# Kernel tuning notes

Hardware: AMD Instinct MI355X
Metric: run time of the kernel (lower is better)

Reference implementation:

```python
import jax, jax.numpy as jnp
import numpy as np

EPS = 1e-5

def _conv3x3(x, w, b):
    # x: [B,C,H,W], w: [O,I,3,3], b: [O]; padding=1 preserves HxW
    y = jax.lax.conv_general_dilated(
        x, w, window_strides=(1, 1), padding=((1, 1), (1, 1)),
        dimension_numbers=('NCHW', 'OIHW', 'NCHW'))
    return y + b[None, :, None, None]

def _instance_norm(x):
    # InstanceNorm2d(affine=False): normalize over spatial dims per (sample, channel)
    mu = jnp.mean(x, axis=(2, 3), keepdims=True)
    var = jnp.var(x, axis=(2, 3), keepdims=True)
    return (x - mu) * jax.lax.rsqrt(var + EPS)

def setup_inputs() -> dict:
    key = jax.random.key(0)
    k1, k2, k3 = jax.random.split(key, 3)
    B, Cin, Cout, H, W = 8, 32, 64, 320, 320
    x = jax.random.normal(k1, (B, Cin, H, W), dtype=jnp.float32)
    w1 = jax.random.normal(k2, (Cout, Cin, 3, 3), dtype=jnp.float32) * (1.0 / np.sqrt(Cin * 9))
    b1 = jnp.zeros((Cout,), dtype=jnp.float32)
    w2 = jax.random.normal(k3, (Cout, Cout, 3, 3), dtype=jnp.float32) * (1.0 / np.sqrt(Cout * 9))
    b2 = jnp.zeros((Cout,), dtype=jnp.float32)
    return {"x": x, "w1": w1, "b1": b1, "w2": w2, "b2": b2}

def reference(x, w1, b1, w2, b2):
    # conv1 -> InstanceNorm -> ReLU -> (Dropout p=0 identity)
    h = jax.nn.relu(_instance_norm(_conv3x3(x, w1, b1)))
    # conv2 -> InstanceNorm -> ReLU -> (Dropout p=0 identity)
    out = jax.nn.relu(_instance_norm(_conv3x3(h, w2, b2)))
    return out
```

## Files before the change

### kernel.cpp

```cpp
#include <hip/hip_runtime.h>

#define HH 320
#define WW 320
#define BB 8
static constexpr float EPS = 1e-5f;

typedef __attribute__((ext_vector_type(8))) short bf16x8;
typedef __attribute__((ext_vector_type(4))) float f32x4;

__device__ inline float bf2f(unsigned short u) {
    union { unsigned int i; float f; } v; v.i = ((unsigned int)u) << 16; return v.f;
}
__device__ inline unsigned short f2bf(float f) {
    union { float f; unsigned int i; } v; v.f = f;
    unsigned int r = v.i + 0x7fffu + ((v.i >> 16) & 1u);
    return (unsigned short)(r >> 16);
}
__device__ inline void glds16(const void* g, void* l) {
    __builtin_amdgcn_global_load_lds(
        (const __attribute__((address_space(1))) unsigned int*)g,
        (__attribute__((address_space(3))) unsigned int*)l, 16, 0, 0);
}

__global__ __launch_bounds__(256) void prep_hwc(const float* __restrict__ in,
                                                unsigned short* __restrict__ out)
{
    __shared__ float sT[32][65];
    const int tid = threadIdx.x;
    const int x0  = blockIdx.x * 64;
    const int y   = blockIdx.y;
    const int b   = blockIdx.z;
    for (int e = tid; e < 32 * 64; e += 256) {
        int c = e >> 6, x = e & 63;
        sT[c][x] = in[(((size_t)(b * 32 + c) * HH) + y) * WW + x0 + x];
    }
    __syncthreads();
    for (int e = tid; e < 64 * 32; e += 256) {
        int x = e >> 5, c = e & 31;
        out[((((size_t)b * HH + y) * WW) + x0 + x) * 32 + c] = f2bf(sT[c][x]);
    }
}

__global__ __launch_bounds__(256) void wprep_swz(const float* __restrict__ w1,
                                                 const float* __restrict__ w2,
                                                 unsigned short* __restrict__ wt1,
                                                 unsigned short* __restrict__ wt2)
{
    int i = blockIdx.x * 256 + threadIdx.x;
    if (i < 2304) {
        int s = i & 3, oc = (i >> 2) & 63, kk = i >> 8;
        int icq = s ^ ((oc >> 1) & 3);
        const float* src = w1 + ((size_t)oc * 32 + icq * 8) * 9 + kk;
        unsigned short pk[8];
#pragma unroll
        for (int j = 0; j < 8; ++j) pk[j] = f2bf(src[j * 9]);
        *(bf16x8*)&wt1[(size_t)i * 8] = *(bf16x8*)pk;
    }
    if (i < 4608) {
        int icc = i / 2304, u = i - icc * 2304;
        int s = u & 3, oc = (u >> 2) & 63, kk = u >> 8;
        int icq = s ^ ((oc >> 1) & 3);
        const float* src = w2 + ((size_t)oc * 64 + icc * 32 + icq * 8) * 9 + kk;
        unsigned short pk[8];
#pragma unroll
        for (int j = 0; j < 8; ++j) pk[j] = f2bf(src[j * 9]);
        *(bf16x8*)&wt2[(size_t)i * 8] = *(bf16x8*)pk;
    }
}

template<int CIN, int NORM>
__global__ __launch_bounds__(256, 2) void conv_mfma(
    const unsigned short* __restrict__ in_hwc,
    const float2* __restrict__ stats_in,
    const unsigned short* __restrict__ wt,
    const float* __restrict__ bias,
    unsigned short* __restrict__ out_hwc,
    float2* __restrict__ partials)
{
    constexpr int ICC = CIN / 32;

    __shared__ __align__(16) unsigned short sA[6 * 264 * 8];
    __shared__ __align__(16) unsigned short sW[2304 * 8];
    __shared__ float sRedS[256];
    __shared__ float sRedSS[256];
    __shared__ float2 sStats[64];

    const int tid = threadIdx.x;
    const int x0  = blockIdx.x * 64;
    const int y0  = blockIdx.y * 4;
    const int b   = blockIdx.z;
    const int w   = tid >> 6;
    const int l   = tid & 63;
    const int lm  = l & 15;
    const int g   = l >> 4;

    if (NORM) {
        if (tid < 64) sStats[tid] = stats_in[b * 64 + tid];
    }

    f32x4 acc[4][4];
#pragma unroll
    for (int fx = 0; fx < 4; ++fx)
#pragma unroll
        for (int fn = 0; fn < 4; ++fn)
            acc[fx][fn] = (f32x4){0.f, 0.f, 0.f, 0.f};

    for (int icc = 0; icc < ICC; ++icc) {
        __syncthreads();

        {
            const unsigned short* wsrc = wt + (size_t)icc * 2304 * 8;
            const int base = w * 576;
#pragma unroll
            for (int i = 0; i < 9; ++i)
                glds16(wsrc + (size_t)(base + i * 64 + l) * 8,
                       sW + (size_t)(base + i * 64) * 8);
        }

        if (NORM == 0) {
            for (int r = w; r < 6; r += 4) {
                int gy = y0 + r - 1;
                unsigned short* ldsrow = sA + r * 2112;
                if ((unsigned)gy < HH) {
                    const unsigned short* rowbase =
                        in_hwc + ((size_t)(b * HH + gy) * WW) * CIN + icc * 32;
#pragma unroll
                    for (int i = 0; i < 4; ++i) {
                        int u  = 4 + i * 64 + l;
                        int x  = u >> 2;
                        int cs = (u & 3) ^ ((x >> 1) & 3);
                        glds16(rowbase + (size_t)(x0 + x - 1) * CIN + cs * 8,
                               ldsrow + (size_t)(4 + i * 64) * 8);
                    }
                } else {
                    for (int u2 = l; u2 < 264; u2 += 64)
                        *(bf16x8*)(ldsrow + u2 * 8) = (bf16x8){0,0,0,0,0,0,0,0};
                }
            }
            if (tid < 48) {
                int icq = tid & 3, side = (tid >> 2) & 1, r = tid >> 3;
                int xs = side ? 65 : 0;
                int gy = y0 + r - 1, gx = x0 + xs - 1;
                bf16x8 v = (bf16x8){0,0,0,0,0,0,0,0};
                if ((unsigned)gy < HH && (unsigned)gx < WW)
                    v = *(const bf16x8*)&in_hwc[(((size_t)(b * HH + gy) * WW) + gx) * CIN + icc * 32 + icq * 8];
                *(bf16x8*)&sA[(r * 264 + xs * 4 + icq) * 8] = v;
            }
        } else {
#pragma unroll
            for (int k = 0; k < 7; ++k) {
                int e = tid + k * 256;
                if (e < 1584) {
                    int r = e / 264, rem = e - r * 264;
                    int x = rem >> 2, icq = rem & 3;
                    int gy = y0 + r - 1, gx = x0 + x - 1;
                    bf16x8 v = (bf16x8){0,0,0,0,0,0,0,0};
                    if ((unsigned)gy < HH && (unsigned)gx < WW)
                        v = *(const bf16x8*)&in_hwc[(((size_t)(b * HH + gy) * WW) + gx) * CIN + icc * 32 + icq * 8];
                    unsigned short res[8];
#pragma unroll
                    for (int j = 0; j < 8; ++j) {
                        float2 ms = sStats[icc * 32 + icq * 8 + j];
                        res[j] = f2bf(fmaxf((bf2f(((unsigned short*)&v)[j]) - ms.x) * ms.y, 0.f));
                    }
                    *(bf16x8*)&sA[(r * 264 + x * 4 + (icq ^ ((x >> 1) & 3))) * 8] = *(bf16x8*)res;
                }
            }
        }
        __syncthreads();

#pragma unroll
        for (int kk = 0; kk < 9; ++kk) {
            const int ky = kk / 3, kx = kk - ky * 3;
            bf16x8 af[4], bfr[4];
#pragma unroll
            for (int fx = 0; fx < 4; ++fx) {
                int xl = fx * 16 + lm + kx;
                int u  = (xl * 4 + g) ^ ((xl >> 1) & 3);
                af[fx] = *(const bf16x8*)&sA[((w + ky) * 264 + u) * 8];
            }
#pragma unroll
            for (int fn = 0; fn < 4; ++fn) {
                int ocr = fn * 16 + lm;
                int p   = (kk * 64 + ocr) * 4 + (g ^ ((ocr >> 1) & 3));
                bfr[fn] = *(const bf16x8*)&sW[p * 8];
            }
#pragma unroll
            for (int fn = 0; fn < 4; ++fn)
#pragma unroll
                for (int fx = 0; fx < 4; ++fx)
                    acc[fx][fn] = __builtin_amdgcn_mfma_f32_16x16x32_bf16(
                        bfr[fn], af[fx], acc[fx][fn], 0, 0, 0);
        }
    }

    const int row = y0 + w;
#pragma unroll
    for (int fo = 0; fo < 4; ++fo) {
        float4 b4 = *(const float4*)&bias[fo * 16 + g * 4];
        float bb[4] = {b4.x, b4.y, b4.z, b4.w};
        float sj[4] = {0,0,0,0}, qj[4] = {0,0,0,0};
#pragma unroll
        for (int fp = 0; fp < 4; ++fp) {
            unsigned short pk[4];
#pragma unroll
            for (int j = 0; j < 4; ++j) {
                float v = acc[fp][fo][j] + bb[j];
                sj[j] += v; qj[j] += v * v;
                pk[j] = f2bf(v);
            }
            *(short4*)&out_hwc[(((size_t)b * HH + row) * WW + x0 + fp * 16 + lm) * 64 + fo * 16 + g * 4] =
                *(short4*)pk;
        }
#pragma unroll
        for (int m = 1; m <= 8; m <<= 1)
#pragma unroll
            for (int j = 0; j < 4; ++j) {
                sj[j] += __shfl_xor(sj[j], m);
                qj[j] += __shfl_xor(qj[j], m);
            }
        if (lm == 0) {
#pragma unroll
            for (int j = 0; j < 4; ++j) {
                sRedS [w * 64 + fo * 16 + g * 4 + j] = sj[j];
                sRedSS[w * 64 + fo * 16 + g * 4 + j] = qj[j];
            }
        }
    }
    __syncthreads();
    if (tid < 64) {
        float S = 0.f, SS = 0.f;
#pragma unroll
        for (int q = 0; q < 4; ++q) { S += sRedS[q * 64 + tid]; SS += sRedSS[q * 64 + tid]; }
        partials[((size_t)b * 400 + blockIdx.y * 5 + blockIdx.x) * 64 + tid] = make_float2(S, SS);
    }
}

__global__ __launch_bounds__(256) void reduce_stats(const float2* __restrict__ partials,
                                                    float2* __restrict__ stats)
{
    const int b  = blockIdx.x;
    const int oc = threadIdx.x & 63;
    const int q  = threadIdx.x >> 6;
    float s = 0.f, ss = 0.f;
    for (int i = q; i < 400; i += 4) {
        float2 p = partials[((size_t)b * 400 + i) * 64 + oc];
        s += p.x; ss += p.y;
    }
    __shared__ float2 red[4][64];
    red[q][oc] = make_float2(s, ss);
    __syncthreads();
    if (threadIdx.x < 64) {
        float S = 0.f, SS = 0.f;
#pragma unroll
        for (int k = 0; k < 4; ++k) { S += red[k][threadIdx.x].x; SS += red[k][threadIdx.x].y; }
        const float n = (float)(HH * WW);
        float mean = S / n;
        float var  = fmaxf(SS / n - mean * mean, 0.f);
        stats[b * 64 + threadIdx.x] = make_float2(mean, rsqrtf(var + EPS));
    }
}

__global__ __launch_bounds__(256) void finalize_t(const unsigned short* __restrict__ h2,
                                                  const float2* __restrict__ stats,
                                                  float* __restrict__ out)
{
    __shared__ float2 sSt[64];
    const int tid = threadIdx.x;
    const int b   = blockIdx.z;
    if (tid < 64) sSt[tid] = stats[b * 64 + tid];
    __syncthreads();
    const int r   = tid >> 6;
    const int px  = tid & 63;
    const int row = blockIdx.y * 4 + r;
    const int x   = blockIdx.x * 64 + px;
    const unsigned short* src = h2 + ((size_t)(b * HH + row) * WW + x) * 64;
    bf16x8 v[8];
#pragma unroll
    for (int cq = 0; cq < 8; ++cq) v[cq] = *(const bf16x8*)(src + cq * 8);
#pragma unroll
    for (int cq = 0; cq < 8; ++cq)
#pragma unroll
        for (int j = 0; j < 8; ++j) {
            int c = cq * 8 + j;
            float2 ms = sSt[c];
            float f = fmaxf((bf2f(((unsigned short*)&v[cq])[j]) - ms.x) * ms.y, 0.f);
            out[((size_t)(b * 64 + c) * HH + row) * WW + x] = f;
        }
}

extern "C" void kernel_launch(void* const* d_in, const int* in_sizes, int n_in,
                              void* d_out, int out_size, void* d_ws, size_t ws_size,
                              hipStream_t stream)
{
    const float* x  = (const float*)d_in[0];
    const float* w1 = (const float*)d_in[1];
    const float* b1 = (const float*)d_in[2];
    const float* w2 = (const float*)d_in[3];
    const float* b2 = (const float*)d_in[4];
    float* out = (float*)d_out;

    char* ws = (char*)d_ws;
    unsigned short* h    = (unsigned short*)ws;
    float2* partials     = (float2*)(ws + 104857600);
    float2* stats1       = (float2*)(ws + 104857600 + 1638400);
    float2* stats2       = (float2*)(ws + 104857600 + 1638400 + 4096);
    unsigned short* reg2 = (unsigned short*)(ws + 104857600 + 1638400 + 8192);
    unsigned short* x_hwc = reg2;
    unsigned short* h2    = reg2;

    unsigned short* wt2 = (unsigned short*)((char*)d_out + 209715200 - 73728);
    unsigned short* wt1 = (unsigned short*)((char*)d_out + 209715200 - 73728 - 36864);

    dim3 cgrid(5, 80, BB);

    wprep_swz<<<18, 256, 0, stream>>>(w1, w2, wt1, wt2);
    prep_hwc<<<dim3(5, HH, BB), 256, 0, stream>>>(x, x_hwc);

    conv_mfma<32, 0><<<cgrid, 256, 0, stream>>>(x_hwc, nullptr, wt1, b1, h, partials);
    reduce_stats<<<BB, 256, 0, stream>>>(partials, stats1);
    conv_mfma<64, 1><<<cgrid, 256, 0, stream>>>(h, stats1, wt2, b2, h2, partials);
    reduce_stats<<<BB, 256, 0, stream>>>(partials, stats2);
    finalize_t<<<dim3(5, 80, BB), 256, 0, stream>>>(h2, stats2, out);
}
```

Baseline: 339.7 us.

## Add ring-buffered conv1 kernel processing 16 rows per block with row reuse

Adds a dedicated conv1 kernel in which each block computes 16 output rows using a 10-slot LDS ring of input rows. Weights are loaded once per block, and each new 4-row step stages only the rows it still needs while computing the current ones. This replaces the 4-row-per-block conv1, which reloaded 6 input rows and the full weight tile for every block. The trade-offs are a quarter as many blocks (800), a larger LDS footprint, and a reduce_stats call that now takes the partial count as a parameter.

```diff
diff --git a/kernel.cpp b/kernel.cpp
--- a/kernel.cpp
+++ b/kernel.cpp
@@ -68,6 +68,165 @@
     }
 }
 
+__global__ __launch_bounds__(256, 2) void conv1_ring(
+    const unsigned short* __restrict__ in_hwc,
+    const unsigned short* __restrict__ wt,
+    const float* __restrict__ bias,
+    unsigned short* __restrict__ out_hwc,
+    float2* __restrict__ partials)
+{
+    __shared__ __align__(16) unsigned short sA[10 * 264 * 8];
+    __shared__ __align__(16) unsigned short sW[2304 * 8];
+    __shared__ float sRedS[256];
+    __shared__ float sRedSS[256];
+
+    const int tid = threadIdx.x;
+    const int x0  = blockIdx.x * 64;
+    const int yb  = blockIdx.y * 16;
+    const int b   = blockIdx.z;
+    const int w   = tid >> 6;
+    const int l   = tid & 63;
+    const int lm  = l & 15;
+    const int g   = l >> 4;
+
+    {
+        const int base = w * 576;
+#pragma unroll
+        for (int i = 0; i < 9; ++i)
+            glds16(wt + (size_t)(base + i * 64 + l) * 8,
+                   sW + (size_t)(base + i * 64) * 8);
+    }
+
+    auto stage_row = [&](int rl, int slot) {
+        int gy = yb - 1 + rl;
+        unsigned short* ldsrow = sA + slot * 2112;
+        if ((unsigned)gy < HH) {
+            const unsigned short* rowbase = in_hwc + ((size_t)(b * HH + gy) * WW) * 32;
+#pragma unroll
+            for (int i = 0; i < 4; ++i) {
+                int u  = 4 + i * 64 + l;
+                int x  = u >> 2;
+                int cs = (u & 3) ^ ((x >> 1) & 3);
+                glds16(rowbase + (size_t)(x0 + x - 1) * 32 + cs * 8,
+                       ldsrow + (size_t)(4 + i * 64) * 8);
+            }
+            if (l < 8) {
+                int icq = l & 3, side = l >> 2;
+                int xs = side ? 65 : 0;
+                int gx = x0 + xs - 1;
+                bf16x8 v = (bf16x8){0,0,0,0,0,0,0,0};
+                if ((unsigned)gx < WW)
+                    v = *(const bf16x8*)&in_hwc[(((size_t)(b * HH + gy) * WW) + gx) * 32 + icq * 8];
+                *(bf16x8*)(ldsrow + (xs * 4 + icq) * 8) = v;
+            }
+        } else {
+            for (int u2 = l; u2 < 264; u2 += 64)
+                *(bf16x8*)(ldsrow + u2 * 8) = (bf16x8){0,0,0,0,0,0,0,0};
+        }
+    };
+
+    f32x4 acc[4][4];
+#pragma unroll
+    for (int fp = 0; fp < 4; ++fp)
+#pragma unroll
+        for (int fo = 0; fo < 4; ++fo)
+            acc[fp][fo] = (f32x4){0.f, 0.f, 0.f, 0.f};
+
+    float bb[4][4];
+#pragma unroll
+    for (int fo = 0; fo < 4; ++fo) {
+        float4 b4 = *(const float4*)&bias[fo * 16 + g * 4];
+        bb[fo][0] = b4.x; bb[fo][1] = b4.y; bb[fo][2] = b4.z; bb[fo][3] = b4.w;
+    }
+    float sjA[4][4] = {}, qjA[4][4] = {};
+
+    stage_row(w, w);
+    if (w < 2) stage_row(4 + w, 4 + w);
+    __syncthreads();
+
+    auto step = [&](int t, bool do_stage) {
+        if (do_stage) {
+            int rl = 4 * (t + 1) + 2 + w;
+            int slot = rl - (rl >= 10 ? 10 : 0);
+            stage_row(rl, slot);
+        }
+#pragma unroll
+        for (int kk = 0; kk < 9; ++kk) {
+            const int ky = kk / 3, kx = kk - ky * 3;
+            int rl = 4 * t + w + ky;
+            int slot = rl - (rl >= 10 ? 10 : 0);
+            const unsigned short* rowp = sA + slot * 2112;
+            bf16x8 af[4], bfr[4];
+#pragma unroll
+            for (int fp = 0; fp < 4; ++fp) {
+                int xl = fp * 16 + lm + kx;
+                int u  = (xl * 4 + g) ^ ((xl >> 1) & 3);
+                af[fp] = *(const bf16x8*)(rowp + u * 8);
+            }
+#pragma unroll
+            for (int fo = 0; fo < 4; ++fo) {
+                int ocr = fo * 16 + lm;
+                int p   = (kk * 64 + ocr) * 4 + (g ^ ((ocr >> 1) & 3));
+                bfr[fo] = *(const bf16x8*)&sW[p * 8];
+            }
+#pragma unroll
+            for (int fo = 0; fo < 4; ++fo)
+#pragma unroll
+                for (int fp = 0; fp < 4; ++fp)
+                    acc[fp][fo] = __builtin_amdgcn_mfma_f32_16x16x32_bf16(
+                        bfr[fo], af[fp], acc[fp][fo], 0, 0, 0);
+        }
+        const int row = yb + 4 * t + w;
+#pragma unroll
+        for (int fo = 0; fo < 4; ++fo) {
+#pragma unroll
+            for (int fp = 0; fp < 4; ++fp) {
+                unsigned short pk[4];
+#pragma unroll
+                for (int j = 0; j < 4; ++j) {
+                    float v = acc[fp][fo][j] + bb[fo][j];
+                    sjA[fo][j] += v; qjA[fo][j] += v * v;
+                    pk[j] = f2bf(v);
+                }
+                *(short4*)&out_hwc[(((size_t)b * HH + row) * WW + x0 + fp * 16 + lm) * 64 + fo * 16 + g * 4] =
+                    *(short4*)pk;
+                acc[fp][fo] = (f32x4){0.f, 0.f, 0.f, 0.f};
+            }
+        }
+        __syncthreads();
+    };
+
+    step(0, true);
+    step(1, true);
+    step(2, true);
+    step(3, false);
+
+#pragma unroll
+    for (int fo = 0; fo < 4; ++fo) {
+#pragma unroll
+        for (int m = 1; m <= 8; m <<= 1)
+#pragma unroll
+            for (int j = 0; j < 4; ++j) {
+                sjA[fo][j] += __shfl_xor(sjA[fo][j], m);
+                qjA[fo][j] += __shfl_xor(qjA[fo][j], m);
+            }
+        if (lm == 0) {
+#pragma unroll
+            for (int j = 0; j < 4; ++j) {
+                sRedS [w * 64 + fo * 16 + g * 4 + j] = sjA[fo][j];
+                sRedSS[w * 64 + fo * 16 + g * 4 + j] = qjA[fo][j];
+            }
+        }
+    }
+    __syncthreads();
+    if (tid < 64) {
+        float S = 0.f, SS = 0.f;
+#pragma unroll
+        for (int q = 0; q < 4; ++q) { S += sRedS[q * 64 + tid]; SS += sRedSS[q * 64 + tid]; }
+        partials[((size_t)b * 100 + blockIdx.y * 5 + blockIdx.x) * 64 + tid] = make_float2(S, SS);
+    }
+}
+
 template<int CIN, int NORM>
 __global__ __launch_bounds__(256, 2) void conv_mfma(
     const unsigned short* __restrict__ in_hwc,
@@ -107,7 +266,6 @@
 
     for (int icc = 0; icc < ICC; ++icc) {
         __syncthreads();
-
         {
             const unsigned short* wsrc = wt + (size_t)icc * 2304 * 8;
             const int base = w * 576;
@@ -116,7 +274,6 @@
                 glds16(wsrc + (size_t)(base + i * 64 + l) * 8,
                        sW + (size_t)(base + i * 64) * 8);
         }
-
         if (NORM == 0) {
             for (int r = w; r < 6; r += 4) {
                 int gy = y0 + r - 1;
@@ -198,14 +355,14 @@
 #pragma unroll
     for (int fo = 0; fo < 4; ++fo) {
         float4 b4 = *(const float4*)&bias[fo * 16 + g * 4];
-        float bb[4] = {b4.x, b4.y, b4.z, b4.w};
+        float bbv[4] = {b4.x, b4.y, b4.z, b4.w};
         float sj[4] = {0,0,0,0}, qj[4] = {0,0,0,0};
 #pragma unroll
         for (int fp = 0; fp < 4; ++fp) {
             unsigned short pk[4];
 #pragma unroll
             for (int j = 0; j < 4; ++j) {
-                float v = acc[fp][fo][j] + bb[j];
+                float v = acc[fp][fo][j] + bbv[j];
                 sj[j] += v; qj[j] += v * v;
                 pk[j] = f2bf(v);
             }
@@ -237,14 +394,14 @@
 }
 
 __global__ __launch_bounds__(256) void reduce_stats(const float2* __restrict__ partials,
-                                                    float2* __restrict__ stats)
+                                                    float2* __restrict__ stats, int count)
 {
     const int b  = blockIdx.x;
     const int oc = threadIdx.x & 63;
     const int q  = threadIdx.x >> 6;
     float s = 0.f, ss = 0.f;
-    for (int i = q; i < 400; i += 4) {
-        float2 p = partials[((size_t)b * 400 + i) * 64 + oc];
+    for (int i = q; i < count; i += 4) {
+        float2 p = partials[((size_t)b * count + i) * 64 + oc];
         s += p.x; ss += p.y;
     }
     __shared__ float2 red[4][64];
@@ -312,14 +469,12 @@
     unsigned short* wt2 = (unsigned short*)((char*)d_out + 209715200 - 73728);
     unsigned short* wt1 = (unsigned short*)((char*)d_out + 209715200 - 73728 - 36864);
 
-    dim3 cgrid(5, 80, BB);
-
     wprep_swz<<<18, 256, 0, stream>>>(w1, w2, wt1, wt2);
     prep_hwc<<<dim3(5, HH, BB), 256, 0, stream>>>(x, x_hwc);
 
-    conv_mfma<32, 0><<<cgrid, 256, 0, stream>>>(x_hwc, nullptr, wt1, b1, h, partials);
-    reduce_stats<<<BB, 256, 0, stream>>>(partials, stats1);
-    conv_mfma<64, 1><<<cgrid, 256, 0, stream>>>(h, stats1, wt2, b2, h2, partials);
-    reduce_stats<<<BB, 256, 0, stream>>>(partials, stats2);
+    conv1_ring<<<dim3(5, 20, BB), 256, 0, stream>>>(x_hwc, wt1, b1, h, partials);
+    reduce_stats<<<BB, 256, 0, stream>>>(partials, stats1, 100);
+    conv_mfma<64, 1><<<dim3(5, 80, BB), 256, 0, stream>>>(h, stats1, wt2, b2, h2, partials);
+    reduce_stats<<<BB, 256, 0, stream>>>(partials, stats2, 400);
     finalize_t<<<dim3(5, 80, BB), 256, 0, stream>>>(h2, stats2, out);
 }
```

Measured after the change: 332.6 us. 2.1% less time.

## Fold instance-norm scale into per-sample conv2 weights and split weight staging by kernel row

Applied to the files above, without the earlier changes.

Adds a wfold kernel that scales conv2 weights by each input channel's inverse std for each sample and folds the mean into a per-sample bias. Conv2's input transform then reduces to max(x, mu), with out-of-bounds padding set to mu, which removes the subtract and multiply per element. The conv kernel now stages weights one kernel row at a time, shrinking LDS use so launch bounds can rise to 4 blocks per CU; it also adds s_setprio around the MFMA loops and uses packed bf16 conversions. The cost is per-sample weight copies, extra barriers per input-channel chunk, and extra rounding because the folded weights are re-quantised to bf16.

```diff
diff --git a/kernel.cpp b/kernel.cpp
--- a/kernel.cpp
+++ b/kernel.cpp
@@ -15,6 +15,11 @@
     union { float f; unsigned int i; } v; v.f = f;
     unsigned int r = v.i + 0x7fffu + ((v.i >> 16) & 1u);
     return (unsigned short)(r >> 16);
+}
+__device__ inline unsigned int cvtpk(float a, float b) {
+    unsigned int r;
+    asm volatile("v_cvt_pk_bf16_f32 %0, %1, %2" : "=v"(r) : "v"(a), "v"(b));
+    return r;
 }
 __device__ inline void glds16(const void* g, void* l) {
     __builtin_amdgcn_global_load_lds(
@@ -68,8 +73,50 @@
     }
 }
 
+__global__ __launch_bounds__(256) void wfold(const unsigned short* __restrict__ wt2,
+                                             const float* __restrict__ b2,
+                                             const float2* __restrict__ stats1,
+                                             unsigned short* __restrict__ wt2b,
+                                             float* __restrict__ bias2b)
+{
+    __shared__ float sMu[64], sR[64];
+    __shared__ float sBias[256];
+    const int b = blockIdx.x, tid = threadIdx.x;
+    if (tid < 64) {
+        float2 ms = stats1[b * 64 + tid];
+        sMu[tid] = bf2f(f2bf(ms.x));
+        sR[tid]  = ms.y;
+    }
+    __syncthreads();
+    const int oc = tid & 63, rep = tid >> 6;
+    float bsum = 0.f;
+    for (int cs = rep * 2; cs < rep * 2 + 2; ++cs) {
+        int icc = cs >> 2, s = cs & 3;
+        int icq = s ^ ((oc >> 1) & 3);
+        for (int kk = 0; kk < 9; ++kk) {
+            size_t u = (size_t)icc * 2304 + kk * 256 + oc * 4 + s;
+            bf16x8 v = *(const bf16x8*)&wt2[u * 8];
+            unsigned short o8[8];
+#pragma unroll
+            for (int j = 0; j < 8; ++j) {
+                int ic = icc * 32 + icq * 8 + j;
+                unsigned short wb = f2bf(bf2f(((unsigned short*)&v)[j]) * sR[ic]);
+                o8[j] = wb;
+                bsum += bf2f(wb) * sMu[ic];
+            }
+            *(bf16x8*)&wt2b[((size_t)b * 4608 + u) * 8] = *(bf16x8*)o8;
+        }
+    }
+    sBias[tid] = bsum;
+    __syncthreads();
+    if (tid < 64) {
+        float t = sBias[tid] + sBias[tid + 64] + sBias[tid + 128] + sBias[tid + 192];
+        bias2b[b * 64 + tid] = b2[tid] - t;
+    }
+}
+
 template<int CIN, int NORM>
-__global__ __launch_bounds__(256, 2) void conv_mfma(
+__global__ __launch_bounds__(256, 4) void conv_mfma(
     const unsigned short* __restrict__ in_hwc,
     const float2* __restrict__ stats_in,
     const unsigned short* __restrict__ wt,
@@ -79,11 +126,13 @@
 {
     constexpr int ICC = CIN / 32;
 
-    __shared__ __align__(16) unsigned short sA[6 * 264 * 8];
-    __shared__ __align__(16) unsigned short sW[2304 * 8];
-    __shared__ float sRedS[256];
-    __shared__ float sRedSS[256];
-    __shared__ float2 sStats[64];
+    __shared__ __align__(16) char smem[38912];
+    unsigned short* sA    = (unsigned short*)smem;
+    unsigned short* sW    = (unsigned short*)(smem + 25344);
+    float*          sMaxMu= (float*)(smem + 37632);
+    unsigned short* sMuBf = (unsigned short*)(smem + 37888);
+    float* sRedS  = (float*)smem;
+    float* sRedSS = (float*)(smem + 1024);
 
     const int tid = threadIdx.x;
     const int x0  = blockIdx.x * 64;
@@ -94,28 +143,27 @@
     const int lm  = l & 15;
     const int g   = l >> 4;
 
+    const unsigned short* wtb = NORM ? wt + (size_t)b * 4608 * 8 : wt;
+    const float* biasb        = NORM ? bias + b * 64 : bias;
+
     if (NORM) {
-        if (tid < 64) sStats[tid] = stats_in[b * 64 + tid];
+        if (tid < 64) {
+            float2 ms = stats_in[b * 64 + tid];
+            unsigned short mb = f2bf(ms.x);
+            sMuBf[tid]  = mb;
+            sMaxMu[tid] = bf2f(mb);
+        }
     }
 
     f32x4 acc[4][4];
 #pragma unroll
-    for (int fx = 0; fx < 4; ++fx)
-#pragma unroll
-        for (int fn = 0; fn < 4; ++fn)
-            acc[fx][fn] = (f32x4){0.f, 0.f, 0.f, 0.f};
+    for (int fp = 0; fp < 4; ++fp)
+#pragma unroll
+        for (int fo = 0; fo < 4; ++fo)
+            acc[fp][fo] = (f32x4){0.f, 0.f, 0.f, 0.f};
 
     for (int icc = 0; icc < ICC; ++icc) {
         __syncthreads();
-
-        {
-            const unsigned short* wsrc = wt + (size_t)icc * 2304 * 8;
-            const int base = w * 576;
-#pragma unroll
-            for (int i = 0; i < 9; ++i)
-                glds16(wsrc + (size_t)(base + i * 64 + l) * 8,
-                       sW + (size_t)(base + i * 64) * 8);
-        }
 
         if (NORM == 0) {
             for (int r = w; r < 6; r += 4) {
@@ -154,63 +202,83 @@
                     int r = e / 264, rem = e - r * 264;
                     int x = rem >> 2, icq = rem & 3;
                     int gy = y0 + r - 1, gx = x0 + x - 1;
-                    bf16x8 v = (bf16x8){0,0,0,0,0,0,0,0};
-                    if ((unsigned)gy < HH && (unsigned)gx < WW)
-                        v = *(const bf16x8*)&in_hwc[(((size_t)(b * HH + gy) * WW) + gx) * CIN + icc * 32 + icq * 8];
-                    unsigned short res[8];
-#pragma unroll
-                    for (int j = 0; j < 8; ++j) {
-                        float2 ms = sStats[icc * 32 + icq * 8 + j];
-                        res[j] = f2bf(fmaxf((bf2f(((unsigned short*)&v)[j]) - ms.x) * ms.y, 0.f));
+                    int c0 = icc * 32 + icq * 8;
+                    unsigned int w4[4];
+                    if ((unsigned)gy < HH && (unsigned)gx < WW) {
+                        bf16x8 v = *(const bf16x8*)&in_hwc[(((size_t)(b * HH + gy) * WW) + gx) * CIN + c0];
+#pragma unroll
+                        for (int jp = 0; jp < 4; ++jp) {
+                            float f0 = fmaxf(bf2f(((unsigned short*)&v)[2 * jp]),     sMaxMu[c0 + 2 * jp]);
+                            float f1 = fmaxf(bf2f(((unsigned short*)&v)[2 * jp + 1]), sMaxMu[c0 + 2 * jp + 1]);
+                            w4[jp] = cvtpk(f0, f1);
+                        }
+                    } else {
+#pragma unroll
+                        for (int jp = 0; jp < 4; ++jp)
+                            w4[jp] = (unsigned int)sMuBf[c0 + 2 * jp] |
+                                     ((unsigned int)sMuBf[c0 + 2 * jp + 1] << 16);
                     }
-                    *(bf16x8*)&sA[(r * 264 + x * 4 + (icq ^ ((x >> 1) & 3))) * 8] = *(bf16x8*)res;
+                    *(uint4*)&sA[(r * 264 + x * 4 + (icq ^ ((x >> 1) & 3))) * 8] =
+                        make_uint4(w4[0], w4[1], w4[2], w4[3]);
                 }
             }
         }
-        __syncthreads();
-
-#pragma unroll
-        for (int kk = 0; kk < 9; ++kk) {
-            const int ky = kk / 3, kx = kk - ky * 3;
-            bf16x8 af[4], bfr[4];
-#pragma unroll
-            for (int fx = 0; fx < 4; ++fx) {
-                int xl = fx * 16 + lm + kx;
-                int u  = (xl * 4 + g) ^ ((xl >> 1) & 3);
-                af[fx] = *(const bf16x8*)&sA[((w + ky) * 264 + u) * 8];
-            }
-#pragma unroll
-            for (int fn = 0; fn < 4; ++fn) {
-                int ocr = fn * 16 + lm;
-                int p   = (kk * 64 + ocr) * 4 + (g ^ ((ocr >> 1) & 3));
-                bfr[fn] = *(const bf16x8*)&sW[p * 8];
-            }
-#pragma unroll
-            for (int fn = 0; fn < 4; ++fn)
-#pragma unroll
-                for (int fx = 0; fx < 4; ++fx)
-                    acc[fx][fn] = __builtin_amdgcn_mfma_f32_16x16x32_bf16(
-                        bfr[fn], af[fx], acc[fx][fn], 0, 0, 0);
-        }
-    }
+
+#pragma unroll
+        for (int kt = 0; kt < 3; ++kt) {
+            if (kt > 0) __syncthreads();
+            {
+                const unsigned short* wsrc = wtb + ((size_t)icc * 2304 + kt * 768) * 8;
+#pragma unroll
+                for (int k = 0; k < 3; ++k)
+                    glds16(wsrc + (size_t)(k * 256 + w * 64 + l) * 8,
+                           sW + (size_t)(k * 256 + w * 64) * 8);
+            }
+            __syncthreads();
+
+            __builtin_amdgcn_s_setprio(1);
+#pragma unroll
+            for (int kx = 0; kx < 3; ++kx) {
+                bf16x8 af[4], bfr[4];
+#pragma unroll
+                for (int fp = 0; fp < 4; ++fp) {
+                    int xl = fp * 16 + lm + kx;
+                    int u  = (xl * 4 + g) ^ ((xl >> 1) & 3);
+                    af[fp] = *(const bf16x8*)&sA[((w + kt) * 264 + u) * 8];
+                }
+#pragma unroll
+                for (int fo = 0; fo < 4; ++fo) {
+                    int ocr = fo * 16 + lm;
+                    int p   = (kx * 64 + ocr) * 4 + (g ^ ((ocr >> 1) & 3));
+                    bfr[fo] = *(const bf16x8*)&sW[p * 8];
+                }
+#pragma unroll
+                for (int fo = 0; fo < 4; ++fo)
+#pragma unroll
+                    for (int fp = 0; fp < 4; ++fp)
+                        acc[fp][fo] = __builtin_amdgcn_mfma_f32_16x16x32_bf16(
+                            bfr[fo], af[fp], acc[fp][fo], 0, 0, 0);
+            }
+            __builtin_amdgcn_s_setprio(0);
+        }
+    }
+
+    __syncthreads();
 
     const int row = y0 + w;
 #pragma unroll
     for (int fo = 0; fo < 4; ++fo) {
-        float4 b4 = *(const float4*)&bias[fo * 16 + g * 4];
+        float4 b4 = *(const float4*)&biasb[fo * 16 + g * 4];
         float bb[4] = {b4.x, b4.y, b4.z, b4.w};
         float sj[4] = {0,0,0,0}, qj[4] = {0,0,0,0};
 #pragma unroll
         for (int fp = 0; fp < 4; ++fp) {
-            unsigned short pk[4];
-#pragma unroll
-            for (int j = 0; j < 4; ++j) {
-                float v = acc[fp][fo][j] + bb[j];
-                sj[j] += v; qj[j] += v * v;
-                pk[j] = f2bf(v);
-            }
-            *(short4*)&out_hwc[(((size_t)b * HH + row) * WW + x0 + fp * 16 + lm) * 64 + fo * 16 + g * 4] =
-                *(short4*)pk;
+            float v0 = acc[fp][fo][0] + bb[0], v1 = acc[fp][fo][1] + bb[1];
+            float v2 = acc[fp][fo][2] + bb[2], v3 = acc[fp][fo][3] + bb[3];
+            sj[0] += v0; qj[0] += v0 * v0;  sj[1] += v1; qj[1] += v1 * v1;
+            sj[2] += v2; qj[2] += v2 * v2;  sj[3] += v3; qj[3] += v3 * v3;
+            uint2 st = make_uint2(cvtpk(v0, v1), cvtpk(v2, v3));
+            *(uint2*)&out_hwc[(((size_t)b * HH + row) * WW + x0 + fp * 16 + lm) * 64 + fo * 16 + g * 4] = st;
         }
 #pragma unroll
         for (int m = 1; m <= 8; m <<= 1)
@@ -237,14 +305,14 @@
 }
 
 __global__ __launch_bounds__(256) void reduce_stats(const float2* __restrict__ partials,
-                                                    float2* __restrict__ stats)
+                                                    float2* __restrict__ stats, int count)
 {
     const int b  = blockIdx.x;
     const int oc = threadIdx.x & 63;
     const int q  = threadIdx.x >> 6;
     float s = 0.f, ss = 0.f;
-    for (int i = q; i < 400; i += 4) {
-        float2 p = partials[((size_t)b * 400 + i) * 64 + oc];
+    for (int i = q; i < count; i += 4) {
+        float2 p = partials[((size_t)b * count + i) * 64 + oc];
         s += p.x; ss += p.y;
     }
     __shared__ float2 red[4][64];
@@ -309,8 +377,11 @@
     unsigned short* x_hwc = reg2;
     unsigned short* h2    = reg2;
 
-    unsigned short* wt2 = (unsigned short*)((char*)d_out + 209715200 - 73728);
-    unsigned short* wt1 = (unsigned short*)((char*)d_out + 209715200 - 73728 - 36864);
+    char* ob = (char*)d_out + 209715200;
+    float*          bias2b = (float*)(ob - 2048);
+    unsigned short* wt2b   = (unsigned short*)(ob - 2048 - 589824);
+    unsigned short* wt2    = (unsigned short*)(ob - 2048 - 589824 - 73728);
+    unsigned short* wt1    = (unsigned short*)(ob - 2048 - 589824 - 73728 - 36864);
 
     dim3 cgrid(5, 80, BB);
 
@@ -318,8 +389,9 @@
     prep_hwc<<<dim3(5, HH, BB), 256, 0, stream>>>(x, x_hwc);
 
     conv_mfma<32, 0><<<cgrid, 256, 0, stream>>>(x_hwc, nullptr, wt1, b1, h, partials);
-    reduce_stats<<<BB, 256, 0, stream>>>(partials, stats1);
-    conv_mfma<64, 1><<<cgrid, 256, 0, stream>>>(h, stats1, wt2, b2, h2, partials);
-    reduce_stats<<<BB, 256, 0, stream>>>(partials, stats2);
+    reduce_stats<<<BB, 256, 0, stream>>>(partials, stats1, 400);
+    wfold<<<BB, 256, 0, stream>>>(wt2, b2, stats1, wt2b, bias2b);
+    conv_mfma<64, 1><<<cgrid, 256, 0, stream>>>(h, stats1, wt2b, bias2b, h2, partials);
+    reduce_stats<<<BB, 256, 0, stream>>>(partials, stats2, 400);
     finalize_t<<<dim3(5, 80, BB), 256, 0, stream>>>(h2, stats2, out);
 }
```

Result: slower. 412.7 us (+21.5%).
